# Performance work log

Hardware: AMD Instinct MI355X
Metric: run time of the kernel (lower is better)

Reference implementation:

```python
import jax, jax.numpy as jnp
import numpy as np

EMBED_DIM = 1024
HEAD_SIZE = 64
BATCH = 8
SEQ = 2048


def setup_inputs() -> dict:
    key = jax.random.key(0)
    k1, k2, k3, k4 = jax.random.split(key, 4)
    x = jax.random.normal(k1, (BATCH, SEQ, EMBED_DIM), dtype=jnp.float32)
    # Dense(use_bias=False) kernels: [in, out]
    scale = 1.0 / np.sqrt(EMBED_DIM)
    Wq = jax.random.normal(k2, (EMBED_DIM, HEAD_SIZE), dtype=jnp.float32) * scale
    Wk = jax.random.normal(k3, (EMBED_DIM, HEAD_SIZE), dtype=jnp.float32) * scale
    Wv = jax.random.normal(k4, (EMBED_DIM, HEAD_SIZE), dtype=jnp.float32) * scale
    return {"x": x, "Wq": Wq, "Wk": Wk, "Wv": Wv}


def reference(x, Wq, Wk, Wv):
    B, S, E = x.shape
    q = jnp.einsum("bse,eh->bsh", x, Wq)
    k = jnp.einsum("bse,eh->bsh", x, Wk)
    v = jnp.einsum("bse,eh->bsh", x, Wv)
    # scores scaled by embedding_dim**-0.5 (as in the original code)
    w = jnp.einsum("bqh,bkh->bqk", q, k) * (E ** -0.5)
    causal = jnp.tril(jnp.ones((S, S), dtype=bool))  # True on/below diag
    w = jnp.where(causal, w, -jnp.inf)
    w = jax.nn.softmax(w, axis=-1)
    # dropout is identity at inference
    return jnp.einsum("bqk,bkh->bqh", w, v)
```

## Files before the change

### kernel.cpp

```cpp
#include <hip/hip_runtime.h>
#include <hip/hip_bf16.h>


#define BATCH 8
#define SEQ   2048
#define EMB   1024
#define HD    64
#define ROWS  (BATCH*SEQ)
#define NTOT  192

typedef __attribute__((ext_vector_type(8))) short short8;
typedef __attribute__((ext_vector_type(4))) float floatx4;

static __device__ __forceinline__ short f2bf(float f) {
  union { __hip_bfloat16 h; short s; } u;
  u.h = __float2bfloat16(f);
  return u.s;
}

__global__ __launch_bounds__(256) void wt_kernel(
    const float* __restrict__ Wq, const float* __restrict__ Wk,
    const float* __restrict__ Wv, short* __restrict__ Wt) {
  const int i = blockIdx.x * 256 + threadIdx.x;
  const int np = i % NTOT;
  const int c4 = i / NTOT;
  const float* __restrict__ W = (np < 64) ? Wq : ((np < 128) ? Wk : Wv);
  const int n = np & 63;
  short4 o;
  o.x = f2bf(W[(c4 * 4 + 0) * HD + n]);
  o.y = f2bf(W[(c4 * 4 + 1) * HD + n]);
  o.z = f2bf(W[(c4 * 4 + 2) * HD + n]);
  o.w = f2bf(W[(c4 * 4 + 3) * HD + n]);
  *(short4*)(Wt + (size_t)np * EMB + c4 * 4) = o;
}

__global__ __launch_bounds__(256, 2) void proj_kernel(
    const float* __restrict__ x, const short* __restrict__ Wt,
    short* __restrict__ qb, short* __restrict__ kb, short* __restrict__ vtb) {
  __shared__ floatx4 red[2][12][64];

  const int t = threadIdx.x, lane = t & 63, w = t >> 6;
  const int lo = lane & 15, quad = lane >> 4;
  const int m0 = blockIdx.x * 16;
  const int k0 = w * 256;

  const float* __restrict__ xr = x + (size_t)(m0 + lo) * EMB + k0 + quad * 8;
  const short* __restrict__ wr = Wt + (size_t)lo * EMB + k0 + quad * 8;

  floatx4 acc[12];
#pragma unroll
  for (int nt = 0; nt < 12; ++nt) acc[nt] = (floatx4){0.f, 0.f, 0.f, 0.f};

  float4 a[8][2];
#pragma unroll
  for (int ks = 0; ks < 8; ++ks) {
    a[ks][0] = *(const float4*)(xr + ks * 32);
    a[ks][1] = *(const float4*)(xr + ks * 32 + 4);
  }

#pragma unroll
  for (int ks = 0; ks < 8; ++ks) {
    short8 bfr[12];
#pragma unroll
    for (int nt = 0; nt < 12; ++nt)
      bfr[nt] = *(const short8*)(wr + ks * 32 + (size_t)nt * 16 * EMB);
    short8 af;
    af[0] = f2bf(a[ks][0].x); af[1] = f2bf(a[ks][0].y);
    af[2] = f2bf(a[ks][0].z); af[3] = f2bf(a[ks][0].w);
    af[4] = f2bf(a[ks][1].x); af[5] = f2bf(a[ks][1].y);
    af[6] = f2bf(a[ks][1].z); af[7] = f2bf(a[ks][1].w);
#pragma unroll
    for (int nt = 0; nt < 12; ++nt)
      acc[nt] = __builtin_amdgcn_mfma_f32_16x16x32_bf16(af, bfr[nt], acc[nt], 0, 0, 0);
  }

  if (w >= 2) {
#pragma unroll
    for (int nt = 0; nt < 12; ++nt) red[w - 2][nt][lane] = acc[nt];
  }
  __syncthreads();
  if (w < 2) {
#pragma unroll
    for (int nt = 0; nt < 12; ++nt) acc[nt] += red[w][nt][lane];
    if (w == 0) {
#pragma unroll
      for (int nt = 6; nt < 12; ++nt) red[0][nt - 6][lane] = acc[nt];
    } else {
#pragma unroll
      for (int nt = 0; nt < 6; ++nt) red[1][nt][lane] = acc[nt];
    }
  }
  __syncthreads();

  if (w < 2) {
    const int bb = m0 >> 11;
    const int s0 = (m0 & (SEQ - 1)) + quad * 4;
    const int rowb = m0 + quad * 4;
    if (w == 0) {
      floatx4 fin[6];
#pragma unroll
      for (int nt = 0; nt < 6; ++nt) fin[nt] = acc[nt] + red[1][nt][lane];
#pragma unroll
      for (int nt = 0; nt < 4; ++nt)
#pragma unroll
        for (int r = 0; r < 4; ++r)
          qb[(size_t)(rowb + r) * HD + nt * 16 + lo] = f2bf(fin[nt][r] * 0.03125f);
#pragma unroll
      for (int nt = 4; nt < 6; ++nt)
#pragma unroll
        for (int r = 0; r < 4; ++r)
          kb[(size_t)(rowb + r) * HD + (nt - 4) * 16 + lo] = f2bf(fin[nt][r]);
    } else {
      floatx4 fin[6];
#pragma unroll
      for (int nt = 0; nt < 6; ++nt) fin[nt] = acc[nt + 6] + red[0][nt][lane];
#pragma unroll
      for (int nt = 0; nt < 2; ++nt)
#pragma unroll
        for (int r = 0; r < 4; ++r)
          kb[(size_t)(rowb + r) * HD + (nt + 2) * 16 + lo] = f2bf(fin[nt][r]);
#pragma unroll
      for (int nt = 2; nt < 6; ++nt) {
        const int col = (nt - 2) * 16 + lo;
        short4 sv = make_short4(f2bf(fin[nt][0]), f2bf(fin[nt][1]),
                                f2bf(fin[nt][2]), f2bf(fin[nt][3]));
        *(short4*)(vtb + ((size_t)bb * HD + col) * SEQ + s0) = sv;
      }
    }
  }
}

#define KSTR 72
#define PSTR 40

__global__ __launch_bounds__(256, 2) void attn_kernel(
    const short* __restrict__ qb, const short* __restrict__ kb,
    const short* __restrict__ vtb, float* __restrict__ out) {
  __shared__ __align__(16) short Ks[2][64 * KSTR];
  __shared__ __align__(16) short Vs[2][64 * KSTR];
  __shared__ __align__(16) short Ps[4][16 * PSTR];
  __shared__ __align__(16) floatx4 Red[2][5][64];

  const int b = blockIdx.y;
  const int bx = blockIdx.x;
  const int qx = (bx & 1) ? (63 - (bx >> 1)) : (bx >> 1);
  const int q0 = qx * 32;
  const int t = threadIdx.x, lane = t & 63, w = t >> 6;
  const int wr = w >> 1, wk = w & 1;
  const int lo = lane & 15, quad = lane >> 4;

  const short* qp = qb + ((size_t)b * SEQ + q0 + wr * 16 + lo) * HD + quad * 8;
  const short8 qf0 = *(const short8*)(qp);
  const short8 qf1 = *(const short8*)(qp + 32);

  const int r0 = t >> 3, c0 = (t & 7) * 8;
  const int r1 = r0 + 32;
  const short* __restrict__ kgb = kb + (size_t)b * SEQ * HD;
  const short* __restrict__ vgb = vtb + (size_t)b * HD * SEQ;

  floatx4 acc[4];
  float lsum[4] = {0.f, 0.f, 0.f, 0.f};
#pragma unroll
  for (int nt = 0; nt < 4; ++nt) acc[nt] = (floatx4){0.f, 0.f, 0.f, 0.f};

  {
    short8 k0v = *(const short8*)(kgb + (size_t)r0 * HD + c0);
    short8 k1v = *(const short8*)(kgb + (size_t)r1 * HD + c0);
    short8 v0v = *(const short8*)(vgb + (size_t)r0 * SEQ + c0);
    short8 v1v = *(const short8*)(vgb + (size_t)r1 * SEQ + c0);
    *(short8*)(&Ks[0][r0 * KSTR + c0]) = k0v;
    *(short8*)(&Ks[0][r1 * KSTR + c0]) = k1v;
    *(short8*)(&Vs[0][r0 * KSTR + c0]) = v0v;
    *(short8*)(&Vs[0][r1 * KSTR + c0]) = v1v;
  }

  const int niter = q0 / 64 + 1;
  for (int it = 0; it < niter; ++it) {
    const int j0 = it * 64;
    const int buf = it & 1;
    __syncthreads();

    short8 kfr[2][2], vfr[4];
#pragma unroll
    for (int n2 = 0; n2 < 2; ++n2) {
      const short* kr = &Ks[buf][(wk * 32 + n2 * 16 + lo) * KSTR + quad * 8];
      kfr[n2][0] = *(const short8*)(kr);
      kfr[n2][1] = *(const short8*)(kr + 32);
    }
#pragma unroll
    for (int nt = 0; nt < 4; ++nt)
      vfr[nt] = *(const short8*)(&Vs[buf][(nt * 16 + lo) * KSTR + wk * 32 + quad * 8]);

    short8 nk0, nk1, nv0, nv1;
    const bool more = (it + 1 < niter);
    if (more) {
      const int jn = j0 + 64;
      nk0 = *(const short8*)(kgb + (size_t)(jn + r0) * HD + c0);
      nk1 = *(const short8*)(kgb + (size_t)(jn + r1) * HD + c0);
      nv0 = *(const short8*)(vgb + (size_t)r0 * SEQ + jn + c0);
      nv1 = *(const short8*)(vgb + (size_t)r1 * SEQ + jn + c0);
    }

    floatx4 s0 = (floatx4){0.f, 0.f, 0.f, 0.f};
    floatx4 s1 = (floatx4){0.f, 0.f, 0.f, 0.f};
    s0 = __builtin_amdgcn_mfma_f32_16x16x32_bf16(qf0, kfr[0][0], s0, 0, 0, 0);
    s0 = __builtin_amdgcn_mfma_f32_16x16x32_bf16(qf1, kfr[0][1], s0, 0, 0, 0);
    s1 = __builtin_amdgcn_mfma_f32_16x16x32_bf16(qf0, kfr[1][0], s1, 0, 0, 0);
    s1 = __builtin_amdgcn_mfma_f32_16x16x32_bf16(qf1, kfr[1][1], s1, 0, 0, 0);

    const bool diag = (j0 + 64 > q0);
    const int rowb = q0 + wr * 16 + quad * 4;
    short* Pw = Ps[w];
#pragma unroll
    for (int r = 0; r < 4; ++r) {
      float e0 = __expf(s0[r]);
      float e1 = __expf(s1[r]);
      if (diag) {
        const int key0 = j0 + wk * 32 + lo;
        e0 = (key0 <= rowb + r) ? e0 : 0.f;
        e1 = (key0 + 16 <= rowb + r) ? e1 : 0.f;
      }
      lsum[r] += e0 + e1;
      Pw[(quad * 4 + r) * PSTR + lo] = f2bf(e0);
      Pw[(quad * 4 + r) * PSTR + 16 + lo] = f2bf(e1);
    }
    const short8 pf = *(const short8*)(&Pw[lo * PSTR + quad * 8]);
#pragma unroll
    for (int nt = 0; nt < 4; ++nt)
      acc[nt] = __builtin_amdgcn_mfma_f32_16x16x32_bf16(pf, vfr[nt], acc[nt], 0, 0, 0);

    if (more) {
      const int nb = buf ^ 1;
      *(short8*)(&Ks[nb][r0 * KSTR + c0]) = nk0;
      *(short8*)(&Ks[nb][r1 * KSTR + c0]) = nk1;
      *(short8*)(&Vs[nb][r0 * KSTR + c0]) = nv0;
      *(short8*)(&Vs[nb][r1 * KSTR + c0]) = nv1;
    }
  }

#pragma unroll
  for (int d = 1; d < 16; d <<= 1) {
#pragma unroll
    for (int r = 0; r < 4; ++r) lsum[r] += __shfl_xor(lsum[r], d);
  }

  if (wk == 1) {
#pragma unroll
    for (int nt = 0; nt < 4; ++nt) Red[wr][nt][lane] = acc[nt];
    Red[wr][4][lane] = (floatx4){lsum[0], lsum[1], lsum[2], lsum[3]};
  }
  __syncthreads();
  if (wk == 0) {
    const floatx4 lp = Red[wr][4][lane];
    const int rowb = q0 + wr * 16 + quad * 4;
#pragma unroll
    for (int nt = 0; nt < 4; ++nt) {
      const floatx4 o = acc[nt] + Red[wr][nt][lane];
#pragma unroll
      for (int r = 0; r < 4; ++r)
        out[((size_t)b * SEQ + rowb + r) * HD + nt * 16 + lo] =
            o[r] / (lsum[r] + lp[r]);
    }
  }
}

extern "C" void kernel_launch(void* const* d_in, const int* in_sizes, int n_in,
                              void* d_out, int out_size, void* d_ws, size_t ws_size,
                              hipStream_t stream) {
  const float* x  = (const float*)d_in[0];
  const float* Wq = (const float*)d_in[1];
  const float* Wk = (const float*)d_in[2];
  const float* Wv = (const float*)d_in[3];
  float* out = (float*)d_out;
  short* ws = (short*)d_ws;
  short* qbp = ws;
  short* kbp = ws + (size_t)ROWS * HD;
  short* vtp = ws + (size_t)2 * ROWS * HD;
  short* Wt  = ws + (size_t)3 * ROWS * HD;

  wt_kernel<<<dim3(NTOT), 256, 0, stream>>>(Wq, Wk, Wv, Wt);
  proj_kernel<<<dim3(ROWS / 16), 256, 0, stream>>>(x, Wt, qbp, kbp, vtp);
  attn_kernel<<<dim3(SEQ / 32, BATCH), 256, 0, stream>>>(qbp, kbp, vtp, out);
}
```

Baseline: 175.4 us.

## Restructure QKV projection to split N across waves with LDS-staged, double-buffered x tiles

The projection kernel no longer splits the K dimension across the four waves and reduces partial sums through shared memory. Each block now covers 32 rows. Each wave owns 3 of the 12 output column tiles and loops over the full K in 32-wide steps. The x tile is converted to bf16 once, held in a double-buffered LDS tile that all waves share, and the next x and W chunks are prefetched during the current MFMAs. This removes the cross-wave reduction and repeated x conversion, but adds a barrier on every one of 32 K steps, and each wave keeps fewer MFMAs in flight per step.

```diff
diff --git a/kernel.cpp b/kernel.cpp
--- a/kernel.cpp
+++ b/kernel.cpp
@@ -34,97 +34,89 @@
   *(short4*)(Wt + (size_t)np * EMB + c4 * 4) = o;
 }
 
+#define ASTR 40
+
 __global__ __launch_bounds__(256, 2) void proj_kernel(
     const float* __restrict__ x, const short* __restrict__ Wt,
     short* __restrict__ qb, short* __restrict__ kb, short* __restrict__ vtb) {
-  __shared__ floatx4 red[2][12][64];
+  __shared__ __align__(16) short As[2][32 * ASTR];
 
   const int t = threadIdx.x, lane = t & 63, w = t >> 6;
   const int lo = lane & 15, quad = lane >> 4;
-  const int m0 = blockIdx.x * 16;
-  const int k0 = w * 256;
-
-  const float* __restrict__ xr = x + (size_t)(m0 + lo) * EMB + k0 + quad * 8;
-  const short* __restrict__ wr = Wt + (size_t)lo * EMB + k0 + quad * 8;
-
-  floatx4 acc[12];
-#pragma unroll
-  for (int nt = 0; nt < 12; ++nt) acc[nt] = (floatx4){0.f, 0.f, 0.f, 0.f};
-
-  float4 a[8][2];
-#pragma unroll
-  for (int ks = 0; ks < 8; ++ks) {
-    a[ks][0] = *(const float4*)(xr + ks * 32);
-    a[ks][1] = *(const float4*)(xr + ks * 32 + 4);
-  }
-
-#pragma unroll
-  for (int ks = 0; ks < 8; ++ks) {
-    short8 bfr[12];
-#pragma unroll
-    for (int nt = 0; nt < 12; ++nt)
-      bfr[nt] = *(const short8*)(wr + ks * 32 + (size_t)nt * 16 * EMB);
-    short8 af;
-    af[0] = f2bf(a[ks][0].x); af[1] = f2bf(a[ks][0].y);
-    af[2] = f2bf(a[ks][0].z); af[3] = f2bf(a[ks][0].w);
-    af[4] = f2bf(a[ks][1].x); af[5] = f2bf(a[ks][1].y);
-    af[6] = f2bf(a[ks][1].z); af[7] = f2bf(a[ks][1].w);
-#pragma unroll
-    for (int nt = 0; nt < 12; ++nt)
-      acc[nt] = __builtin_amdgcn_mfma_f32_16x16x32_bf16(af, bfr[nt], acc[nt], 0, 0, 0);
-  }
-
-  if (w >= 2) {
-#pragma unroll
-    for (int nt = 0; nt < 12; ++nt) red[w - 2][nt][lane] = acc[nt];
-  }
-  __syncthreads();
-  if (w < 2) {
-#pragma unroll
-    for (int nt = 0; nt < 12; ++nt) acc[nt] += red[w][nt][lane];
-    if (w == 0) {
-#pragma unroll
-      for (int nt = 6; nt < 12; ++nt) red[0][nt - 6][lane] = acc[nt];
-    } else {
-#pragma unroll
-      for (int nt = 0; nt < 6; ++nt) red[1][nt][lane] = acc[nt];
-    }
-  }
-  __syncthreads();
-
-  if (w < 2) {
-    const int bb = m0 >> 11;
-    const int s0 = (m0 & (SEQ - 1)) + quad * 4;
-    const int rowb = m0 + quad * 4;
-    if (w == 0) {
-      floatx4 fin[6];
-#pragma unroll
-      for (int nt = 0; nt < 6; ++nt) fin[nt] = acc[nt] + red[1][nt][lane];
-#pragma unroll
-      for (int nt = 0; nt < 4; ++nt)
+  const int m0 = blockIdx.x * 32;
+
+  const int srow = t >> 3, sc4 = t & 7;
+  const float* __restrict__ xs = x + (size_t)(m0 + srow) * EMB + sc4 * 4;
+
+  const short* __restrict__ wb = Wt + (size_t)(w * 3 * 16 + lo) * EMB + quad * 8;
+
+  floatx4 acc[2][3];
+#pragma unroll
+  for (int mf = 0; mf < 2; ++mf)
+#pragma unroll
+    for (int j = 0; j < 3; ++j) acc[mf][j] = (floatx4){0.f, 0.f, 0.f, 0.f};
+
+  {
+    const float4 xv = *(const float4*)(xs);
+    *(short4*)(&As[0][srow * ASTR + sc4 * 4]) =
+        make_short4(f2bf(xv.x), f2bf(xv.y), f2bf(xv.z), f2bf(xv.w));
+  }
+  short8 b0 = *(const short8*)(wb);
+  short8 b1 = *(const short8*)(wb + (size_t)16 * EMB);
+  short8 b2 = *(const short8*)(wb + (size_t)32 * EMB);
+
+  for (int ks = 0; ks < 32; ++ks) {
+    const int buf = ks & 1;
+    __syncthreads();
+
+    float4 xn;
+    short8 nb0, nb1, nb2;
+    if (ks < 31) {
+      const int ko = (ks + 1) * 32;
+      xn = *(const float4*)(xs + ko);
+      nb0 = *(const short8*)(wb + ko);
+      nb1 = *(const short8*)(wb + ko + (size_t)16 * EMB);
+      nb2 = *(const short8*)(wb + ko + (size_t)32 * EMB);
+    }
+
+    const short8 af0 = *(const short8*)(&As[buf][(lo) * ASTR + quad * 8]);
+    const short8 af1 = *(const short8*)(&As[buf][(16 + lo) * ASTR + quad * 8]);
+
+    acc[0][0] = __builtin_amdgcn_mfma_f32_16x16x32_bf16(af0, b0, acc[0][0], 0, 0, 0);
+    acc[1][0] = __builtin_amdgcn_mfma_f32_16x16x32_bf16(af1, b0, acc[1][0], 0, 0, 0);
+    acc[0][1] = __builtin_amdgcn_mfma_f32_16x16x32_bf16(af0, b1, acc[0][1], 0, 0, 0);
+    acc[1][1] = __builtin_amdgcn_mfma_f32_16x16x32_bf16(af1, b1, acc[1][1], 0, 0, 0);
+    acc[0][2] = __builtin_amdgcn_mfma_f32_16x16x32_bf16(af0, b2, acc[0][2], 0, 0, 0);
+    acc[1][2] = __builtin_amdgcn_mfma_f32_16x16x32_bf16(af1, b2, acc[1][2], 0, 0, 0);
+
+    if (ks < 31) {
+      *(short4*)(&As[buf ^ 1][srow * ASTR + sc4 * 4]) =
+          make_short4(f2bf(xn.x), f2bf(xn.y), f2bf(xn.z), f2bf(xn.w));
+      b0 = nb0; b1 = nb1; b2 = nb2;
+    }
+  }
+
+  const int bb = m0 >> 11;
+  const int sbase = (m0 & (SEQ - 1)) + quad * 4;
+#pragma unroll
+  for (int mf = 0; mf < 2; ++mf) {
+    const int rowb = m0 + mf * 16 + quad * 4;
+#pragma unroll
+    for (int j = 0; j < 3; ++j) {
+      const int nt = w * 3 + j;
+      const floatx4 v = acc[mf][j];
+      if (nt < 4) {
 #pragma unroll
         for (int r = 0; r < 4; ++r)
-          qb[(size_t)(rowb + r) * HD + nt * 16 + lo] = f2bf(fin[nt][r] * 0.03125f);
-#pragma unroll
-      for (int nt = 4; nt < 6; ++nt)
+          qb[(size_t)(rowb + r) * HD + nt * 16 + lo] = f2bf(v[r] * 0.03125f);
+      } else if (nt < 8) {
 #pragma unroll
         for (int r = 0; r < 4; ++r)
-          kb[(size_t)(rowb + r) * HD + (nt - 4) * 16 + lo] = f2bf(fin[nt][r]);
-    } else {
-      floatx4 fin[6];
-#pragma unroll
-      for (int nt = 0; nt < 6; ++nt) fin[nt] = acc[nt + 6] + red[0][nt][lane];
-#pragma unroll
-      for (int nt = 0; nt < 2; ++nt)
-#pragma unroll
-        for (int r = 0; r < 4; ++r)
-          kb[(size_t)(rowb + r) * HD + (nt + 2) * 16 + lo] = f2bf(fin[nt][r]);
-#pragma unroll
-      for (int nt = 2; nt < 6; ++nt) {
-        const int col = (nt - 2) * 16 + lo;
-        short4 sv = make_short4(f2bf(fin[nt][0]), f2bf(fin[nt][1]),
-                                f2bf(fin[nt][2]), f2bf(fin[nt][3]));
-        *(short4*)(vtb + ((size_t)bb * HD + col) * SEQ + s0) = sv;
+          kb[(size_t)(rowb + r) * HD + (nt - 4) * 16 + lo] = f2bf(v[r]);
+      } else {
+        const int col = (nt - 8) * 16 + lo;
+        short4 sv = make_short4(f2bf(v[0]), f2bf(v[1]), f2bf(v[2]), f2bf(v[3]));
+        *(short4*)(vtb + ((size_t)bb * HD + col) * SEQ + sbase + mf * 16) = sv;
       }
     }
   }
@@ -279,6 +271,6 @@
   short* Wt  = ws + (size_t)3 * ROWS * HD;
 
   wt_kernel<<<dim3(NTOT), 256, 0, stream>>>(Wq, Wk, Wv, Wt);
-  proj_kernel<<<dim3(ROWS / 16), 256, 0, stream>>>(x, Wt, qbp, kbp, vtp);
+  proj_kernel<<<dim3(ROWS / 32), 256, 0, stream>>>(x, Wt, qbp, kbp, vtp);
   attn_kernel<<<dim3(SEQ / 32, BATCH), 256, 0, stream>>>(qbp, kbp, vtp, out);
 }
```

Measured after the change: 156.5 us. -10.8%, faster.
